# Performance work log

Measured on AMD Instinct MI355X. Metric: run time of the kernel, lower is better.

## Reference

```python
import jax, jax.numpy as jnp
import numpy as np

NUM_GROUPS = 19  # cityscapes classes; groups in the grouped conv
GATES = 4
SLABS = 4  # hidden slabs per class


def setup_inputs() -> dict:
    key = jax.random.key(0)
    k1, k2, k3, k4, k5 = jax.random.split(key, 5)
    B, H, Wd = 4, 256, 512
    x = jax.random.normal(k1, (B, NUM_GROUPS, H, Wd), dtype=jnp.float32)
    h = jax.random.normal(k2, (B, NUM_GROUPS, SLABS, H, Wd), dtype=jnp.float32)
    c = jax.random.normal(k3, (B, NUM_GROUPS, SLABS, H, Wd), dtype=jnp.float32)
    # Conv2d(95 -> 304, k=3, groups=19): weight (304, 5, 3, 3), bias (304,)
    fan_in = 5 * 3 * 3
    bound = 1.0 / np.sqrt(fan_in)
    W = jax.random.uniform(k4, (4 * NUM_GROUPS * SLABS, 5, 3, 3), minval=-bound, maxval=bound, dtype=jnp.float32)
    b = jax.random.uniform(k5, (4 * NUM_GROUPS * SLABS,), minval=-bound, maxval=bound, dtype=jnp.float32)
    return {"x": x, "h": h, "c": c, "W": W, "b": b}


def reference(x, h, c, W, b):
    B, _, H, Wd = x.shape
    # Strided interleave: channel g*5+0 = x[:,g], g*5+1..4 = h[:,g,0..3]
    xh = jnp.concatenate([x[:, :, None], h], axis=2).reshape(B, NUM_GROUPS * 5, H, Wd)
    A = jax.lax.conv_general_dilated(
        xh, W, window_strides=(1, 1), padding=[(1, 1), (1, 1)],
        feature_group_count=NUM_GROUPS,
        dimension_numbers=("NCHW", "OIHW", "NCHW"))
    A = A + b[None, :, None, None]
    A = A.reshape(B, NUM_GROUPS, GATES, SLABS, H, Wd)
    i = jax.nn.sigmoid(A[:, :, 0])
    f = jax.nn.sigmoid(A[:, :, 1])
    o = jax.nn.sigmoid(A[:, :, 2])
    g = jnp.tanh(A[:, :, 3])
    new_c = f * c + i * g
    new_h = o * jnp.tanh(new_c)
    return (new_h, new_c)
```

## Files before the change

kernel.cpp:

```cpp
#include <hip/hip_runtime.h>
#include <hip/hip_bf16.h>

#define NG      19
#define HEIGHT  256
#define WIDTH   512
#define HW      (HEIGHT*WIDTH)
#define BATCH   4
#define TH      16
#define TW      64
#define HALO_R  18
#define HALO_CU 34
#define CH_U32  (HALO_R*HALO_CU)
#define LDS_U32 (5*CH_U32)
#define ROWB    (HALO_CU*4)
#define CHB     (CH_U32*4)
#define WFRAG_SHORTS (NG*64*16)
#define BIAS_FLOATS  (NG*16)

typedef __attribute__((ext_vector_type(8))) short short8;
typedef __attribute__((ext_vector_type(4))) float f32x4;
typedef __attribute__((ext_vector_type(2))) float f32x2;
typedef __attribute__((ext_vector_type(4))) unsigned int u32x4;

static __device__ __forceinline__ unsigned int bfbits(float f) {
    return (unsigned int)__builtin_bit_cast(unsigned short, __float2bfloat16(f));
}
static __device__ __forceinline__ unsigned int pack2(float lo, float hi) {
    return bfbits(lo) | (bfbits(hi) << 16);
}

__global__ void wxform_kernel(const float* __restrict__ W,
                              const float* __restrict__ b,
                              short* __restrict__ wdst,
                              float* __restrict__ bdst) {
    int i = blockIdx.x * 256 + threadIdx.x;
    if (i < WFRAG_SHORTS) {
        int g   = i / 1024;
        int r   = i & 1023;
        int l   = r >> 4;
        int j   = r & 15;
        int q   = l >> 4;
        int row = l & 15;
        int s    = row >> 2;
        int gate = row & 3;
        int half = j >> 3;
        int jj   = j & 7;
        int m  = 8*half + 2*q + (jj >> 2);
        int kc = jj & 3;
        float wv = 0.0f;
        if (m <= 14 && kc < 3) {
            int ic = m / 3, kr = m % 3;
            int oc = g*16 + gate*4 + s;
            float scale = (gate == 3) ? -2.88539008f : -1.44269504f;
            wv = scale * W[((oc*5 + ic)*3 + kr)*3 + kc];
        }
        wdst[i] = (short)__builtin_bit_cast(unsigned short, __float2bfloat16(wv));
    } else if (i < WFRAG_SHORTS + BIAS_FLOATS) {
        int idx = i - WFRAG_SHORTS;
        int g = idx >> 4;
        int r = idx & 15;
        int s = r >> 2, gate = r & 3;
        float scale = (gate == 3) ? -2.88539008f : -1.44269504f;
        bdst[idx] = scale * b[g*16 + gate*4 + s];
    }
}

__launch_bounds__(256, 6)
__global__ void convlstm_mfma(const float* __restrict__ x,
                              const float* __restrict__ h,
                              const float* __restrict__ c,
                              const short* __restrict__ wfrag,
                              const float* __restrict__ biasp,
                              float* __restrict__ out) {
    __shared__ unsigned int lds0[LDS_U32];
    __shared__ unsigned int lds1[LDS_U32];

    const int t     = threadIdx.x;
    const int bid   = blockIdx.x;
    const int plane = bid >> 7;
    const int tile  = bid & 127;
    const int tr0   = (tile >> 3) * TH;
    const int tc0   = (tile & 7)  * TW;
    const int g     = plane % NG;

    const int w  = t >> 6;
    const int l  = t & 63;
    const int q  = l >> 4;
    const int li = l & 15;

    const int NC_OFF   = BATCH * NG * 4 * HW;
    const int rowbase0 = (plane*4 + q)*HW + (tr0 + w*4)*WIDTH + tc0 + 4*li;

    f32x4 cp[4];
    #pragma unroll
    for (int tr4 = 0; tr4 < 4; ++tr4)
        cp[tr4] = __builtin_nontemporal_load(
            reinterpret_cast<const f32x4*>(c + rowbase0 + tr4*WIDTH));

    const short8* ap = reinterpret_cast<const short8*>(wfrag + (g*64 + l)*16);
    const short8 a_lo = ap[0];
    const short8 a_hi = ap[1];
    const f32x4 bias4 = *reinterpret_cast<const f32x4*>(biasp + g*16 + q*4);

    const float* xb = x + plane * HW;
    const float* hb = h + (plane * 4) * HW;
    const bool lt = (tc0 == 0), rt = (tc0 == 448);

    int r  = t / HALO_CU;
    int j2 = t - r * HALO_CU;
    int ch = 0;

    #pragma unroll
    for (int half = 0; half < 2; ++half) {
        f32x2 pf[6]; float ex[6]; int pidx[6]; bool vld[6];
        #pragma unroll
        for (int k2 = 0; k2 < 6; ++k2) {
            const int k = half*6 + k2;
            const int p = t + 256*k;
            const bool v = (k < 11) ? true : (p < LDS_U32);
            pidx[k2] = p;  vld[k2] = v;
            const int  gr  = tr0 + r - 1;
            const bool rok = v && ((unsigned)gr < HEIGHT);
            const bool pok = rok && !(lt && j2 == 0) && !(rt && j2 == 33);
            const bool eok = rok && !(rt && j2 >= 32);
            const float* bp = (ch == 0) ? xb : (hb + (ch - 1) * HW);
            const int off = gr*WIDTH + tc0 + 2*j2 - 2;
            f32x2 z; z[0] = 0.0f; z[1] = 0.0f;
            pf[k2] = pok ? *reinterpret_cast<const f32x2*>(bp + off) : z;
            ex[k2] = eok ? bp[off + 2] : 0.0f;
            j2 += 18; r += 7;
            if (j2 >= HALO_CU) { j2 -= HALO_CU; r += 1; }
            if (r  >= HALO_R)  { r  -= HALO_R;  ch += 1; }
        }
        #pragma unroll
        for (int k2 = 0; k2 < 6; ++k2) {
            if (vld[k2]) {
                lds0[pidx[k2]] = pack2(pf[k2][0], pf[k2][1]);
                lds1[pidx[k2]] = pack2(pf[k2][1], ex[k2]);
            }
        }
    }

    asm volatile("s_waitcnt lgkmcnt(0)" ::: "memory");
    __builtin_amdgcn_s_barrier();
    asm volatile("" ::: "memory");

    int dbase[4];
    #pragma unroll
    for (int i = 0; i < 4; ++i) {
        int m = (i < 2) ? (2*q + i) : (8 + 2*q + (i - 2));
        if (m > 14) m = 14;
        dbase[i] = ((m/3)*CHB + (m%3)*ROWB + 8*li) >> 2;
    }

    #pragma unroll
    for (int tr4 = 0; tr4 < 4; ++tr4) {
        const int tr  = w*4 + tr4;
        const int drw = tr * (ROWB >> 2);
        const int d0 = dbase[0] + drw, d1 = dbase[1] + drw;
        const int d2 = dbase[2] + drw, d3 = dbase[3] + drw;

        float nh4[4], nc4[4];
        #pragma unroll
        for (int n = 0; n < 4; ++n) {
            u32x4 blo_u, bhi_u;
            if (n == 0) {
                blo_u[0]=lds1[d0];   blo_u[1]=lds1[d0+1]; blo_u[2]=lds1[d1];   blo_u[3]=lds1[d1+1];
                bhi_u[0]=lds1[d2];   bhi_u[1]=lds1[d2+1]; bhi_u[2]=lds1[d3];   bhi_u[3]=lds1[d3+1];
            } else if (n == 1) {
                blo_u[0]=lds0[d0+1]; blo_u[1]=lds0[d0+2]; blo_u[2]=lds0[d1+1]; blo_u[3]=lds0[d1+2];
                bhi_u[0]=lds0[d2+1]; bhi_u[1]=lds0[d2+2]; bhi_u[2]=lds0[d3+1]; bhi_u[3]=lds0[d3+2];
            } else if (n == 2) {
                blo_u[0]=lds1[d0+1]; blo_u[1]=lds1[d0+2]; blo_u[2]=lds1[d1+1]; blo_u[3]=lds1[d1+2];
                bhi_u[0]=lds1[d2+1]; bhi_u[1]=lds1[d2+2]; bhi_u[2]=lds1[d3+1]; bhi_u[3]=lds1[d3+2];
            } else {
                blo_u[0]=lds0[d0+2]; blo_u[1]=lds0[d0+3]; blo_u[2]=lds0[d1+2]; blo_u[3]=lds0[d1+3];
                bhi_u[0]=lds0[d2+2]; bhi_u[1]=lds0[d2+3]; bhi_u[2]=lds0[d3+2]; bhi_u[3]=lds0[d3+3];
            }
            const short8 blo = __builtin_bit_cast(short8, blo_u);
            const short8 bhi = __builtin_bit_cast(short8, bhi_u);

            f32x4 acc = bias4;
            acc = __builtin_amdgcn_mfma_f32_16x16x32_bf16(a_lo, blo, acc, 0, 0, 0);
            acc = __builtin_amdgcn_mfma_f32_16x16x32_bf16(a_hi, bhi, acc, 0, 0, 0);

            const float cv = cp[tr4][n];
            const float u  = __builtin_amdgcn_exp2f(acc[0]);
            const float v  = __builtin_amdgcn_exp2f(acc[1]);
            const float wo = __builtin_amdgcn_exp2f(acc[2]);
            const float z  = __builtin_amdgcn_exp2f(acc[3]);
            const float pu = 1.0f + u,  pv = 1.0f + v;
            const float pw = 1.0f + wo, pz = 1.0f + z;
            const float puz = pu * pz;
            const float r1  = __builtin_amdgcn_rcpf(pv * puz);
            const float nc  = fmaf(cv, puz, (1.0f - z) * pv) * r1;
            const float tt2 = __builtin_amdgcn_exp2f(-2.88539008f * nc);
            const float r2  = __builtin_amdgcn_rcpf(pw * (1.0f + tt2));
            nc4[n] = nc;
            nh4[n] = (1.0f - tt2) * r2;
        }

        const int rowchan = rowbase0 + tr4*WIDTH;
        f32x4 nhv; nhv[0]=nh4[0]; nhv[1]=nh4[1]; nhv[2]=nh4[2]; nhv[3]=nh4[3];
        f32x4 ncv; ncv[0]=nc4[0]; ncv[1]=nc4[1]; ncv[2]=nc4[2]; ncv[3]=nc4[3];
        __builtin_nontemporal_store(nhv, reinterpret_cast<f32x4*>(out + rowchan));
        __builtin_nontemporal_store(ncv, reinterpret_cast<f32x4*>(out + NC_OFF + rowchan));
    }
}

extern "C" void kernel_launch(void* const* d_in, const int* in_sizes, int n_in,
                              void* d_out, int out_size, void* d_ws, size_t ws_size,
                              hipStream_t stream) {
    (void)in_sizes; (void)n_in; (void)out_size; (void)ws_size;
    const float* x = (const float*)d_in[0];
    const float* h = (const float*)d_in[1];
    const float* c = (const float*)d_in[2];
    const float* W = (const float*)d_in[3];
    const float* b = (const float*)d_in[4];
    float* out = (float*)d_out;

    short* wdst = (short*)d_ws;
    float* bdst = (float*)((char*)d_ws + WFRAG_SHORTS * sizeof(short));

    hipLaunchKernelGGL(wxform_kernel,
                       dim3((WFRAG_SHORTS + BIAS_FLOATS + 255) / 256), dim3(256),
                       0, stream, W, b, wdst, bdst);
    hipLaunchKernelGGL(convlstm_mfma, dim3(BATCH * NG * 128), dim3(256),
                       0, stream, x, h, c, (const short*)wdst, bdst, out);
}
```

Before: 140.5 us.

## Drop duplicated shifted LDS copy; build odd-offset fragments with funnel shifts, retile 8x128

Removes the second, pre-shifted LDS buffer and instead reads aligned uint2 pairs from a single bf16-packed buffer, rebuilding the odd-column-offset B fragments in registers with 16-bit funnel shifts. The tile changes from 16x64 to 8x128 and launch bounds move to 8 waves/SIMD occupancy, halving LDS footprint and the extra scalar loads for the halo. This trades fewer LDS stores and loads plus higher occupancy for extra ALU shift work and a larger relative halo in rows.

```diff
diff --git a/kernel.cpp b/kernel.cpp
--- a/kernel.cpp
+++ b/kernel.cpp
@@ -6,14 +6,12 @@
 #define WIDTH   512
 #define HW      (HEIGHT*WIDTH)
 #define BATCH   4
-#define TH      16
-#define TW      64
-#define HALO_R  18
-#define HALO_CU 34
+#define TH      8
+#define TW      128
+#define HALO_R  10
+#define HALO_CU 66
 #define CH_U32  (HALO_R*HALO_CU)
 #define LDS_U32 (5*CH_U32)
-#define ROWB    (HALO_CU*4)
-#define CHB     (CH_U32*4)
 #define WFRAG_SHORTS (NG*64*16)
 #define BIAS_FLOATS  (NG*16)
 
@@ -27,6 +25,9 @@
 }
 static __device__ __forceinline__ unsigned int pack2(float lo, float hi) {
     return bfbits(lo) | (bfbits(hi) << 16);
+}
+static __device__ __forceinline__ unsigned int fsh16(unsigned int hi, unsigned int lo) {
+    return (unsigned int)((((unsigned long long)hi << 32) | lo) >> 16);
 }
 
 __global__ void wxform_kernel(const float* __restrict__ W,
@@ -65,7 +66,7 @@
     }
 }
 
-__launch_bounds__(256, 6)
+__launch_bounds__(256, 8)
 __global__ void convlstm_mfma(const float* __restrict__ x,
                               const float* __restrict__ h,
                               const float* __restrict__ c,
@@ -73,14 +74,13 @@
                               const float* __restrict__ biasp,
                               float* __restrict__ out) {
     __shared__ unsigned int lds0[LDS_U32];
-    __shared__ unsigned int lds1[LDS_U32];
 
     const int t     = threadIdx.x;
     const int bid   = blockIdx.x;
     const int plane = bid >> 7;
     const int tile  = bid & 127;
-    const int tr0   = (tile >> 3) * TH;
-    const int tc0   = (tile & 7)  * TW;
+    const int tr0   = (tile >> 2) * TH;
+    const int tc0   = (tile & 3)  * TW;
     const int g     = plane % NG;
 
     const int w  = t >> 6;
@@ -89,13 +89,15 @@
     const int li = l & 15;
 
     const int NC_OFF   = BATCH * NG * 4 * HW;
-    const int rowbase0 = (plane*4 + q)*HW + (tr0 + w*4)*WIDTH + tc0 + 4*li;
+    const int rowbase0 = (plane*4 + q)*HW + (tr0 + 2*w)*WIDTH + tc0 + 4*li;
 
     f32x4 cp[4];
     #pragma unroll
-    for (int tr4 = 0; tr4 < 4; ++tr4)
-        cp[tr4] = __builtin_nontemporal_load(
-            reinterpret_cast<const f32x4*>(c + rowbase0 + tr4*WIDTH));
+    for (int rr = 0; rr < 2; ++rr)
+        #pragma unroll
+        for (int cc = 0; cc < 2; ++cc)
+            cp[rr*2 + cc] = __builtin_nontemporal_load(
+                reinterpret_cast<const f32x4*>(c + rowbase0 + rr*WIDTH + cc*64));
 
     const short8* ap = reinterpret_cast<const short8*>(wfrag + (g*64 + l)*16);
     const short8 a_lo = ap[0];
@@ -104,7 +106,7 @@
 
     const float* xb = x + plane * HW;
     const float* hb = h + (plane * 4) * HW;
-    const bool lt = (tc0 == 0), rt = (tc0 == 448);
+    const bool lt = (tc0 == 0), rt = (tc0 == 384);
 
     int r  = t / HALO_CU;
     int j2 = t - r * HALO_CU;
@@ -112,32 +114,30 @@
 
     #pragma unroll
     for (int half = 0; half < 2; ++half) {
-        f32x2 pf[6]; float ex[6]; int pidx[6]; bool vld[6];
-        #pragma unroll
-        for (int k2 = 0; k2 < 6; ++k2) {
-            const int k = half*6 + k2;
+        const int NB = half ? 6 : 7;
+        f32x2 pf[7]; int pidx[7]; bool vld[7];
+        #pragma unroll
+        for (int k2 = 0; k2 < 7; ++k2) {
+            if (k2 >= NB) break;
+            const int k = half ? (7 + k2) : k2;
             const int p = t + 256*k;
-            const bool v = (k < 11) ? true : (p < LDS_U32);
+            const bool v = (k < 12) || (t < (LDS_U32 - 12*256));
             pidx[k2] = p;  vld[k2] = v;
             const int  gr  = tr0 + r - 1;
             const bool rok = v && ((unsigned)gr < HEIGHT);
-            const bool pok = rok && !(lt && j2 == 0) && !(rt && j2 == 33);
-            const bool eok = rok && !(rt && j2 >= 32);
+            const bool pok = rok && !(lt && j2 == 0) && !(rt && j2 == 65);
             const float* bp = (ch == 0) ? xb : (hb + (ch - 1) * HW);
             const int off = gr*WIDTH + tc0 + 2*j2 - 2;
             f32x2 z; z[0] = 0.0f; z[1] = 0.0f;
             pf[k2] = pok ? *reinterpret_cast<const f32x2*>(bp + off) : z;
-            ex[k2] = eok ? bp[off + 2] : 0.0f;
-            j2 += 18; r += 7;
+            j2 += 58; r += 3;
             if (j2 >= HALO_CU) { j2 -= HALO_CU; r += 1; }
             if (r  >= HALO_R)  { r  -= HALO_R;  ch += 1; }
         }
         #pragma unroll
-        for (int k2 = 0; k2 < 6; ++k2) {
-            if (vld[k2]) {
-                lds0[pidx[k2]] = pack2(pf[k2][0], pf[k2][1]);
-                lds1[pidx[k2]] = pack2(pf[k2][1], ex[k2]);
-            }
+        for (int k2 = 0; k2 < 7; ++k2) {
+            if (k2 >= NB) break;
+            if (vld[k2]) lds0[pidx[k2]] = pack2(pf[k2][0], pf[k2][1]);
         }
     }
 
@@ -145,66 +145,71 @@
     __builtin_amdgcn_s_barrier();
     asm volatile("" ::: "memory");
 
-    int dbase[4];
+    int cbase[4];
     #pragma unroll
     for (int i = 0; i < 4; ++i) {
         int m = (i < 2) ? (2*q + i) : (8 + 2*q + (i - 2));
         if (m > 14) m = 14;
-        dbase[i] = ((m/3)*CHB + (m%3)*ROWB + 8*li) >> 2;
-    }
-
-    #pragma unroll
-    for (int tr4 = 0; tr4 < 4; ++tr4) {
-        const int tr  = w*4 + tr4;
-        const int drw = tr * (ROWB >> 2);
-        const int d0 = dbase[0] + drw, d1 = dbase[1] + drw;
-        const int d2 = dbase[2] + drw, d3 = dbase[3] + drw;
-
-        float nh4[4], nc4[4];
-        #pragma unroll
-        for (int n = 0; n < 4; ++n) {
-            u32x4 blo_u, bhi_u;
-            if (n == 0) {
-                blo_u[0]=lds1[d0];   blo_u[1]=lds1[d0+1]; blo_u[2]=lds1[d1];   blo_u[3]=lds1[d1+1];
-                bhi_u[0]=lds1[d2];   bhi_u[1]=lds1[d2+1]; bhi_u[2]=lds1[d3];   bhi_u[3]=lds1[d3+1];
-            } else if (n == 1) {
-                blo_u[0]=lds0[d0+1]; blo_u[1]=lds0[d0+2]; blo_u[2]=lds0[d1+1]; blo_u[3]=lds0[d1+2];
-                bhi_u[0]=lds0[d2+1]; bhi_u[1]=lds0[d2+2]; bhi_u[2]=lds0[d3+1]; bhi_u[3]=lds0[d3+2];
-            } else if (n == 2) {
-                blo_u[0]=lds1[d0+1]; blo_u[1]=lds1[d0+2]; blo_u[2]=lds1[d1+1]; blo_u[3]=lds1[d1+2];
-                bhi_u[0]=lds1[d2+1]; bhi_u[1]=lds1[d2+2]; bhi_u[2]=lds1[d3+1]; bhi_u[3]=lds1[d3+2];
-            } else {
-                blo_u[0]=lds0[d0+2]; blo_u[1]=lds0[d0+3]; blo_u[2]=lds0[d1+2]; blo_u[3]=lds0[d1+3];
-                bhi_u[0]=lds0[d2+2]; bhi_u[1]=lds0[d2+3]; bhi_u[2]=lds0[d3+2]; bhi_u[3]=lds0[d3+3];
+        cbase[i] = (m/3)*CH_U32 + (m%3)*HALO_CU + 2*li;
+    }
+
+    #pragma unroll
+    for (int rr = 0; rr < 2; ++rr) {
+        const int tr = 2*w + rr;
+        #pragma unroll
+        for (int cc = 0; cc < 2; ++cc) {
+            const int dadd = tr*HALO_CU + cc*32;
+            uint2 dv[4][2];
+            #pragma unroll
+            for (int i = 0; i < 4; ++i) {
+                const int idx = cbase[i] + dadd;
+                dv[i][0] = *reinterpret_cast<const uint2*>(&lds0[idx]);
+                dv[i][1] = *reinterpret_cast<const uint2*>(&lds0[idx + 2]);
             }
-            const short8 blo = __builtin_bit_cast(short8, blo_u);
-            const short8 bhi = __builtin_bit_cast(short8, bhi_u);
-
-            f32x4 acc = bias4;
-            acc = __builtin_amdgcn_mfma_f32_16x16x32_bf16(a_lo, blo, acc, 0, 0, 0);
-            acc = __builtin_amdgcn_mfma_f32_16x16x32_bf16(a_hi, bhi, acc, 0, 0, 0);
-
-            const float cv = cp[tr4][n];
-            const float u  = __builtin_amdgcn_exp2f(acc[0]);
-            const float v  = __builtin_amdgcn_exp2f(acc[1]);
-            const float wo = __builtin_amdgcn_exp2f(acc[2]);
-            const float z  = __builtin_amdgcn_exp2f(acc[3]);
-            const float pu = 1.0f + u,  pv = 1.0f + v;
-            const float pw = 1.0f + wo, pz = 1.0f + z;
-            const float puz = pu * pz;
-            const float r1  = __builtin_amdgcn_rcpf(pv * puz);
-            const float nc  = fmaf(cv, puz, (1.0f - z) * pv) * r1;
-            const float tt2 = __builtin_amdgcn_exp2f(-2.88539008f * nc);
-            const float r2  = __builtin_amdgcn_rcpf(pw * (1.0f + tt2));
-            nc4[n] = nc;
-            nh4[n] = (1.0f - tt2) * r2;
-        }
-
-        const int rowchan = rowbase0 + tr4*WIDTH;
-        f32x4 nhv; nhv[0]=nh4[0]; nhv[1]=nh4[1]; nhv[2]=nh4[2]; nhv[3]=nh4[3];
-        f32x4 ncv; ncv[0]=nc4[0]; ncv[1]=nc4[1]; ncv[2]=nc4[2]; ncv[3]=nc4[3];
-        __builtin_nontemporal_store(nhv, reinterpret_cast<f32x4*>(out + rowchan));
-        __builtin_nontemporal_store(ncv, reinterpret_cast<f32x4*>(out + NC_OFF + rowchan));
+            float nh4[4], nc4[4];
+            #pragma unroll
+            for (int n = 0; n < 4; ++n) {
+                u32x4 blo_u, bhi_u;
+                #pragma unroll
+                for (int i = 0; i < 4; ++i) {
+                    const unsigned d0 = dv[i][0].x, d1 = dv[i][0].y;
+                    const unsigned d2 = dv[i][1].x, d3 = dv[i][1].y;
+                    unsigned w0, w1;
+                    if (n == 0)      { w0 = fsh16(d1,d0); w1 = fsh16(d2,d1); }
+                    else if (n == 1) { w0 = d1;           w1 = d2;           }
+                    else if (n == 2) { w0 = fsh16(d2,d1); w1 = fsh16(d3,d2); }
+                    else             { w0 = d2;           w1 = d3;           }
+                    if (i < 2) { blo_u[2*i]     = w0; blo_u[2*i+1]     = w1; }
+                    else       { bhi_u[2*(i-2)] = w0; bhi_u[2*(i-2)+1] = w1; }
+                }
+                const short8 blo = __builtin_bit_cast(short8, blo_u);
+                const short8 bhi = __builtin_bit_cast(short8, bhi_u);
+
+                f32x4 acc = bias4;
+                acc = __builtin_amdgcn_mfma_f32_16x16x32_bf16(a_lo, blo, acc, 0, 0, 0);
+                acc = __builtin_amdgcn_mfma_f32_16x16x32_bf16(a_hi, bhi, acc, 0, 0, 0);
+
+                const float cv = cp[rr*2 + cc][n];
+                const float u  = __builtin_amdgcn_exp2f(acc[0]);
+                const float v  = __builtin_amdgcn_exp2f(acc[1]);
+                const float wo = __builtin_amdgcn_exp2f(acc[2]);
+                const float z  = __builtin_amdgcn_exp2f(acc[3]);
+                const float pu = 1.0f + u,  pv = 1.0f + v;
+                const float pw = 1.0f + wo, pz = 1.0f + z;
+                const float puz = pu * pz;
+                const float r1  = __builtin_amdgcn_rcpf(pv * puz);
+                const float nc  = fmaf(cv, puz, (1.0f - z) * pv) * r1;
+                const float tt2 = __builtin_amdgcn_exp2f(-2.88539008f * nc);
+                const float r2  = __builtin_amdgcn_rcpf(pw * (1.0f + tt2));
+                nc4[n] = nc;
+                nh4[n] = (1.0f - tt2) * r2;
+            }
+            const int rowchan = rowbase0 + rr*WIDTH + cc*64;
+            f32x4 nhv; nhv[0]=nh4[0]; nhv[1]=nh4[1]; nhv[2]=nh4[2]; nhv[3]=nh4[3];
+            f32x4 ncv; ncv[0]=nc4[0]; ncv[1]=nc4[1]; ncv[2]=nc4[2]; ncv[3]=nc4[3];
+            __builtin_nontemporal_store(nhv, reinterpret_cast<f32x4*>(out + rowchan));
+            __builtin_nontemporal_store(ncv, reinterpret_cast<f32x4*>(out + NC_OFF + rowchan));
+        }
     }
 }
 
```

Measured after the change: 171.7 us. 22.2% more time.
